# Kernel tuning notes

Hardware: AMD Instinct MI355X
Metric: run time of the kernel (lower is better)

## Reference

```python
import jax, jax.numpy as jnp
import numpy as np


def _tsallis15_probs(x):
    """entmax-1.5 / Tsallis alpha=1.5 mapping over axis=1. x: [n, d] logits."""
    x = (x - jnp.max(x, axis=1, keepdims=True)) * 0.5
    xs = -jnp.sort(-x, axis=1)                       # descending sort  [n, d]
    d = x.shape[1]
    rho = jnp.arange(1, d + 1, dtype=x.dtype)        # 1..d
    mean = jnp.cumsum(xs, axis=1) / rho
    mean_sq = jnp.cumsum(xs * xs, axis=1) / rho
    ss = rho * (mean_sq - mean * mean)
    delta = (1.0 - ss) / rho
    tau = mean - jnp.sqrt(jnp.clip(delta, 0.0))
    support_size = jnp.sum(tau <= xs, axis=1)        # [n]
    tau_star = jnp.take_along_axis(tau, (support_size - 1)[:, None], axis=1)
    y = jnp.clip(x - tau_star, 0.0)
    return y * y                                     # p*, rows sum to 1


def setup_inputs() -> dict:
    key = jax.random.key(0)
    k1, k2 = jax.random.split(key)
    inp = jax.random.normal(k1, (2048, 32000), dtype=jnp.float32)
    target = jax.random.randint(k2, (2048,), 0, 32000, dtype=jnp.int64)
    return {"input": inp, "target": target}


def reference(input, target):
    n = input.shape[0]
    p_star = _tsallis15_probs(input)
    # omega_tsallis15: (1 - sum p^{3/2}) / 0.75 per row
    loss = (1.0 - jnp.sum(p_star * jnp.sqrt(p_star), axis=1)) / 0.75
    # scatter_add(-1) at the target class, then <p* - e_y, x> per row
    pm = p_star.at[jnp.arange(n), target].add(-1.0)
    loss = loss + jnp.einsum('ij,ij->i', pm, input)
    # reduction='elementwise_mean', ignore_index=-100 (<0: no masking)
    return jnp.sum(loss) / n
```

## Files before the change

### kernel.cpp

```cpp
#include <hip/hip_runtime.h>
#include <math.h>

#define BLOCK 1024
#define NWAVES (BLOCK / 64)
#define CAND_CAP 8192

__device__ __forceinline__ float waveReduceMax(float v) {
#pragma unroll
    for (int off = 32; off > 0; off >>= 1)
        v = fmaxf(v, __shfl_down(v, off, 64));
    return v;
}
__device__ __forceinline__ float waveReduceSum(float v) {
#pragma unroll
    for (int off = 32; off > 0; off >>= 1)
        v += __shfl_down(v, off, 64);
    return v;
}

__global__ __launch_bounds__(BLOCK, 8) void tsallis15_kernel(
    const float* __restrict__ x, const int* __restrict__ tgt,
    float* __restrict__ out, int n, int d, float inv_n)
{
    __shared__ float s_cand[CAND_CAP];
    __shared__ float s_red[NWAVES];
    __shared__ int   s_cnt;
    __shared__ float s_bcast;

    const int row  = blockIdx.x;
    const int t    = threadIdx.x;
    const int lane = t & 63;
    const int wave = t >> 6;
    const float* __restrict__ xr = x + (size_t)row * (size_t)d;

    if (t == 0) s_cnt = 0;

    float4 r[8];
#pragma unroll
    for (int i = 0; i < 8; ++i) {
        int e = (i * BLOCK + t) * 4;
        if (e + 4 <= d) {
            r[i] = *reinterpret_cast<const float4*>(xr + e);
        } else {
            float4 v = make_float4(-INFINITY, -INFINITY, -INFINITY, -INFINITY);
            if (e < d)     v.x = xr[e];
            if (e + 1 < d) v.y = xr[e + 1];
            if (e + 2 < d) v.z = xr[e + 2];
            r[i] = v;
        }
    }

    float m = -INFINITY;
#pragma unroll
    for (int i = 0; i < 8; ++i)
        m = fmaxf(m, fmaxf(fmaxf(r[i].x, r[i].y), fmaxf(r[i].z, r[i].w)));
    m = waveReduceMax(m);
    if (lane == 0) s_red[wave] = m;
    __syncthreads();
    if (wave == 0) {
        float v = (lane < NWAVES) ? s_red[lane] : -INFINITY;
        v = waveReduceMax(v);
        if (lane == 0) s_bcast = v;
    }
    __syncthreads();
    const float rowmax = s_bcast;

    const float thr = rowmax - 2.0f;
#pragma unroll
    for (int i = 0; i < 8; ++i) {
        float vals[4] = { r[i].x, r[i].y, r[i].z, r[i].w };
#pragma unroll
        for (int c = 0; c < 4; ++c) {
            float v = vals[c];
            if (v >= thr) {
                int idx = atomicAdd(&s_cnt, 1);
                if (idx < CAND_CAP) s_cand[idx] = (v - rowmax) * 0.5f;
            }
        }
    }
    __syncthreads();

    if (wave == 0) {
        const int k = min(s_cnt, CAND_CAP);

        float lo = -1.0f, hi = 0.0f;
        for (int it = 0; it < 22; ++it) {
            float tau = 0.5f * (lo + hi);
            float local = 0.0f;
            for (int j = lane; j < k; j += 64) {
                float u = s_cand[j] - tau;
                if (u > 0.0f) local += u * u;
            }
            float tot = waveReduceSum(local);
            tot = __shfl(tot, 0, 64);
            if (tot >= 1.0f) lo = tau; else hi = tau;
        }
        const float tau_b = 0.5f * (lo + hi);

        float s1 = 0.0f, s2 = 0.0f, sc = 0.0f;
        for (int j = lane; j < k; j += 64) {
            float u = s_cand[j];
            if (u > tau_b) { s1 += u; s2 += u * u; sc += 1.0f; }
        }
        s1 = waveReduceSum(s1); s1 = __shfl(s1, 0, 64);
        s2 = waveReduceSum(s2); s2 = __shfl(s2, 0, 64);
        sc = waveReduceSum(sc); sc = __shfl(sc, 0, 64);
        float mean  = s1 / sc;
        float ss    = s2 - s1 * mean;
        float delta = (1.0f - ss) / sc;
        if (delta < 0.0f) delta = 0.0f;
        const float tau_star = mean - sqrtf(delta);

        float p32 = 0.0f, dot = 0.0f;
        for (int j = lane; j < k; j += 64) {
            float u = s_cand[j] - tau_star;
            if (u > 0.0f) {
                float p = u * u;
                p32 += p * u;
                dot += p * (2.0f * s_cand[j] + rowmax);
            }
        }
        p32 = waveReduceSum(p32);
        dot = waveReduceSum(dot);
        if (lane == 0) {
            float xt   = xr[tgt[row]];
            float loss = (1.0f - p32) * (4.0f / 3.0f) + dot - xt;
            atomicAdd(out, loss * inv_n);
        }
    }
}

extern "C" void kernel_launch(void* const* d_in, const int* in_sizes, int n_in,
                              void* d_out, int out_size, void* d_ws, size_t ws_size,
                              hipStream_t stream) {
    const float* x   = (const float*)d_in[0];
    const int*   tgt = (const int*)d_in[1];
    float*       out = (float*)d_out;

    const int n = in_sizes[1];
    const int d = in_sizes[0] / n;

    hipMemsetAsync(out, 0, (size_t)out_size * sizeof(float), stream);
    tsallis15_kernel<<<n, BLOCK, 0, stream>>>(x, tgt, out, n, d, 1.0f / (float)n);
}
```

Baseline: 386.9 us.

## Use wave-aggregated candidate append and register-cached bisection over candidates

Replaces the per-element shared-memory atomicAdd for candidate collection with a ballot/popcount wave-aggregated append, so each wave issues one atomic per element slot instead of one per passing element. Caches up to 12 candidates per lane in registers for the single-wave bisection and final reductions, which removes repeated LDS reads. It also cuts the bisection iterations from 22 to 18, lowers the shared candidate capacity and relaxes the launch bounds occupancy hint. Fewer iterations leave a slightly coarser bracket before the exact tau refinement, and the extra registers may reduce occupancy.

```diff
diff --git a/kernel.cpp b/kernel.cpp
--- a/kernel.cpp
+++ b/kernel.cpp
@@ -3,7 +3,8 @@
 
 #define BLOCK 1024
 #define NWAVES (BLOCK / 64)
-#define CAND_CAP 8192
+#define CAND_CAP 6144
+#define NREG 12
 
 __device__ __forceinline__ float waveReduceMax(float v) {
 #pragma unroll
@@ -18,7 +19,7 @@
     return v;
 }
 
-__global__ __launch_bounds__(BLOCK, 8) void tsallis15_kernel(
+__global__ __launch_bounds__(BLOCK, 4) void tsallis15_kernel(
     const float* __restrict__ x, const int* __restrict__ tgt,
     float* __restrict__ out, int n, int d, float inv_n)
 {
@@ -72,9 +73,16 @@
 #pragma unroll
         for (int c = 0; c < 4; ++c) {
             float v = vals[c];
-            if (v >= thr) {
-                int idx = atomicAdd(&s_cnt, 1);
-                if (idx < CAND_CAP) s_cand[idx] = (v - rowmax) * 0.5f;
+            bool pred = (v >= thr);
+            unsigned long long mask = __ballot(pred);
+            if (mask) {
+                int base;
+                if (lane == 0) base = atomicAdd(&s_cnt, __popcll(mask));
+                base = __shfl(base, 0, 64);
+                if (pred) {
+                    int pos = base + (int)__popcll(mask & ((1ull << lane) - 1ull));
+                    if (pos < CAND_CAP) s_cand[pos] = (v - rowmax) * 0.5f;
+                }
             }
         }
     }
@@ -83,22 +91,39 @@
     if (wave == 0) {
         const int k = min(s_cnt, CAND_CAP);
 
+        float ur[NREG];
+#pragma unroll
+        for (int j = 0; j < NREG; ++j) {
+            int idx = lane + 64 * j;
+            ur[j] = (idx < k) ? s_cand[idx] : -1e30f;
+        }
+
         float lo = -1.0f, hi = 0.0f;
-        for (int it = 0; it < 22; ++it) {
+        for (int it = 0; it < 18; ++it) {
             float tau = 0.5f * (lo + hi);
-            float local = 0.0f;
-            for (int j = lane; j < k; j += 64) {
+            float acc = 0.0f;
+#pragma unroll
+            for (int j = 0; j < NREG; ++j) {
+                float u = ur[j] - tau;
+                acc += (u > 0.0f) ? u * u : 0.0f;
+            }
+            for (int j = 64 * NREG + lane; j < k; j += 64) {
                 float u = s_cand[j] - tau;
-                if (u > 0.0f) local += u * u;
+                if (u > 0.0f) acc += u * u;
             }
-            float tot = waveReduceSum(local);
+            float tot = waveReduceSum(acc);
             tot = __shfl(tot, 0, 64);
             if (tot >= 1.0f) lo = tau; else hi = tau;
         }
         const float tau_b = 0.5f * (lo + hi);
 
         float s1 = 0.0f, s2 = 0.0f, sc = 0.0f;
-        for (int j = lane; j < k; j += 64) {
+#pragma unroll
+        for (int j = 0; j < NREG; ++j) {
+            float u = ur[j];
+            if (u > tau_b) { s1 += u; s2 += u * u; sc += 1.0f; }
+        }
+        for (int j = 64 * NREG + lane; j < k; j += 64) {
             float u = s_cand[j];
             if (u > tau_b) { s1 += u; s2 += u * u; sc += 1.0f; }
         }
@@ -112,12 +137,22 @@
         const float tau_star = mean - sqrtf(delta);
 
         float p32 = 0.0f, dot = 0.0f;
-        for (int j = lane; j < k; j += 64) {
-            float u = s_cand[j] - tau_star;
+#pragma unroll
+        for (int j = 0; j < NREG; ++j) {
+            float u = ur[j] - tau_star;
             if (u > 0.0f) {
                 float p = u * u;
                 p32 += p * u;
-                dot += p * (2.0f * s_cand[j] + rowmax);
+                dot += p * (2.0f * ur[j] + rowmax);
+            }
+        }
+        for (int j = 64 * NREG + lane; j < k; j += 64) {
+            float uc = s_cand[j];
+            float u  = uc - tau_star;
+            if (u > 0.0f) {
+                float p = u * u;
+                p32 += p * u;
+                dot += p * (2.0f * uc + rowmax);
             }
         }
         p32 = waveReduceSum(p32);
```

After: 373.9 us. -3.4%, faster.
